# Kernel optimization log

Measured on AMD Instinct MI355X. Metric: run time of the kernel, lower is better.

Reference implementation:

```python
import jax, jax.numpy as jnp
import numpy as np

B, N, C, K = 2, 4096, 256, 64


def setup_inputs() -> dict:
    key = jax.random.key(0)
    k1, k2, k3, k4, k5, k6 = jax.random.split(key, 6)
    points = jax.random.normal(k1, (B, N, 3), dtype=jnp.float32)  # ~N(0,1) cloud
    point_features = jax.random.normal(k2, (B, N, C), dtype=jnp.float32)
    # proposals: centers inside the cloud, positive box dims, random yaw (unused by mask math)
    centers = jax.random.uniform(k3, (B, K, 3), minval=-1.0, maxval=1.0, dtype=jnp.float32)
    dims = jax.random.uniform(k4, (B, K, 3), minval=0.5, maxval=1.5, dtype=jnp.float32)
    ry = jax.random.uniform(k5, (B, K, 1), minval=-np.pi, maxval=np.pi, dtype=jnp.float32)
    proposals = jnp.concatenate([centers, dims, ry], axis=-1)  # (B,K,7)
    W1 = jax.random.normal(k6, (C, 256), dtype=jnp.float32) * (1.0 / np.sqrt(C))
    b1 = jnp.zeros((256,), dtype=jnp.float32)
    W2 = jax.random.normal(jax.random.fold_in(key, 7), (256, 256), dtype=jnp.float32) * (1.0 / 16.0)
    b2 = jnp.zeros((256,), dtype=jnp.float32)
    return {"points": points, "point_features": point_features, "proposals": proposals,
            "W1": W1, "b1": b1, "W2": W2, "b2": b2}


def reference(points, point_features, proposals, W1, b1, W2, b2):
    # points: (B,N,3), point_features: (B,N,C), proposals: (B,K,7)
    ctr = proposals[..., :3]                      # (B,K,3) cx,cy,cz
    half = proposals[..., 3:6] * 0.5              # (B,K,3) l/2,w/2,h/2
    lo = ctr - half                               # (B,K,3)
    hi = ctr + half
    # point-in-box mask (axis-aligned, strict inequalities as in source): (B,K,N)
    p = points[:, None, :, :]                     # (B,1,N,3)
    mask = jnp.all((p > lo[:, :, None, :]) & (p < hi[:, :, None, :]), axis=-1)
    any_in = jnp.any(mask, axis=-1)               # (B,K)
    # masked max-pool over points: (B,K,N,C) -> (B,K,C)
    neg_inf = jnp.asarray(-jnp.inf, point_features.dtype)
    masked = jnp.where(mask[..., None], point_features[:, None, :, :], neg_inf)
    pooled = jnp.max(masked, axis=2)
    pooled = jnp.where(any_in[..., None], pooled, 0.0)  # empty box -> zeros
    # fc: Linear(C,256) + ReLU + Linear(256,256) + ReLU
    h = jax.nn.relu(jnp.einsum('bkc,cd->bkd', pooled, W1) + b1)
    out = jax.nn.relu(jnp.einsum('bkd,de->bke', h, W2) + b2)
    return out
```

## Files before the change

### kernel.cpp

```cpp
#include <hip/hip_runtime.h>

#define Bn 2
#define Nn 4096
#define Cn 256
#define Kn 64
#define BK (Bn * Kn)

__global__ __launch_bounds__(256) void pool_partial_kernel(
    const float* __restrict__ points,
    const float* __restrict__ feats,
    const float* __restrict__ proposals,
    float* __restrict__ partial,
    int S)
{
    const int bk  = blockIdx.x;
    const int s   = blockIdx.y;
    const int b   = bk / Kn;
    const int tid = threadIdx.x;
    const int seg = Nn / S;
    const int n0  = s * seg;

    __shared__ int s_idx[4096];
    __shared__ int s_count;

    const float* prop = proposals + (size_t)bk * 7;
    const float cx = prop[0], cy = prop[1], cz = prop[2];
    const float hx = prop[3] * 0.5f, hy = prop[4] * 0.5f, hz = prop[5] * 0.5f;
    const float lox = cx - hx, loy = cy - hy, loz = cz - hz;
    const float hix = cx + hx, hiy = cy + hy, hiz = cz + hz;

    if (tid == 0) s_count = 0;
    __syncthreads();

    const float* pts = points + (size_t)b * Nn * 3;
    for (int n = n0 + tid; n < n0 + seg; n += 256) {
        const float px = pts[n * 3 + 0];
        const float py = pts[n * 3 + 1];
        const float pz = pts[n * 3 + 2];
        const bool in = (px > lox) & (px < hix) &
                        (py > loy) & (py < hiy) &
                        (pz > loz) & (pz < hiz);
        if (in) {
            const int pos = atomicAdd(&s_count, 1);
            s_idx[pos] = n;
        }
    }
    __syncthreads();
    const int count = s_count;

    const float* fb = feats + (size_t)b * Nn * Cn;
    float m = -INFINITY;
    int i = 0;
    for (; i + 8 <= count; i += 8) {
        const int a0 = s_idx[i + 0], a1 = s_idx[i + 1];
        const int a2 = s_idx[i + 2], a3 = s_idx[i + 3];
        const int a4 = s_idx[i + 4], a5 = s_idx[i + 5];
        const int a6 = s_idx[i + 6], a7 = s_idx[i + 7];
        const float f0 = fb[(size_t)a0 * Cn + tid];
        const float f1 = fb[(size_t)a1 * Cn + tid];
        const float f2 = fb[(size_t)a2 * Cn + tid];
        const float f3 = fb[(size_t)a3 * Cn + tid];
        const float f4 = fb[(size_t)a4 * Cn + tid];
        const float f5 = fb[(size_t)a5 * Cn + tid];
        const float f6 = fb[(size_t)a6 * Cn + tid];
        const float f7 = fb[(size_t)a7 * Cn + tid];
        m = fmaxf(m, fmaxf(fmaxf(fmaxf(f0, f1), fmaxf(f2, f3)),
                           fmaxf(fmaxf(f4, f5), fmaxf(f6, f7))));
    }
    for (; i < count; ++i) {
        m = fmaxf(m, fb[(size_t)s_idx[i] * Cn + tid]);
    }

    partial[((size_t)bk * S + s) * Cn + tid] = m;
}

__global__ __launch_bounds__(256) void reduce_mlp_kernel(
    const float* __restrict__ partial,
    const float* __restrict__ W1,
    const float* __restrict__ b1,
    const float* __restrict__ W2,
    const float* __restrict__ b2,
    float* __restrict__ out,
    int S)
{
    const int bk  = blockIdx.x;
    const int tid = threadIdx.x;

    __shared__ float s_vec[Cn];

    float m = -INFINITY;
    for (int s = 0; s < S; ++s) {
        m = fmaxf(m, partial[((size_t)bk * S + s) * Cn + tid]);
    }
    if (m == -INFINITY) m = 0.0f;
    s_vec[tid] = m;
    __syncthreads();

    float acc = b1[tid];
    #pragma unroll 16
    for (int c = 0; c < Cn; ++c) {
        acc = fmaf(s_vec[c], W1[c * 256 + tid], acc);
    }
    const float h = fmaxf(acc, 0.0f);
    __syncthreads();
    s_vec[tid] = h;
    __syncthreads();

    float acc2 = b2[tid];
    #pragma unroll 16
    for (int c = 0; c < 256; ++c) {
        acc2 = fmaf(s_vec[c], W2[c * 256 + tid], acc2);
    }
    out[(size_t)bk * 256 + tid] = fmaxf(acc2, 0.0f);
}

extern "C" void kernel_launch(void* const* d_in, const int* in_sizes, int n_in,
                              void* d_out, int out_size, void* d_ws, size_t ws_size,
                              hipStream_t stream) {
    const float* points    = (const float*)d_in[0];
    const float* feats     = (const float*)d_in[1];
    const float* proposals = (const float*)d_in[2];
    const float* W1        = (const float*)d_in[3];
    const float* b1        = (const float*)d_in[4];
    const float* W2        = (const float*)d_in[5];
    const float* b2        = (const float*)d_in[6];
    float* out             = (float*)d_out;
    float* partial         = (float*)d_ws;

    int S = 8;
    while (S > 1 && (size_t)BK * S * Cn * sizeof(float) > ws_size) S >>= 1;

    dim3 grid1(BK, S);
    pool_partial_kernel<<<grid1, 256, 0, stream>>>(points, feats, proposals, partial, S);
    reduce_mlp_kernel<<<BK, 256, 0, stream>>>(partial, W1, b1, W2, b2, out, S);
}
```

Measured before the change: 90.74 us.

## Fuse pooling and MLP into one 1024-thread kernel per proposal

```diff
diff --git a/kernel.cpp b/kernel.cpp
--- a/kernel.cpp
+++ b/kernel.cpp
@@ -5,23 +5,35 @@
 #define Cn 256
 #define Kn 64
 #define BK (Bn * Kn)
+#define NW 16
+#define BT 1024
 
-__global__ __launch_bounds__(256) void pool_partial_kernel(
+__device__ __forceinline__ float4 max4(float4 a, float4 b) {
+    return make_float4(fmaxf(a.x, b.x), fmaxf(a.y, b.y),
+                       fmaxf(a.z, b.z), fmaxf(a.w, b.w));
+}
+
+__global__ __launch_bounds__(BT) void fused_roi_kernel(
     const float* __restrict__ points,
     const float* __restrict__ feats,
     const float* __restrict__ proposals,
-    float* __restrict__ partial,
-    int S)
+    const float* __restrict__ W1,
+    const float* __restrict__ b1,
+    const float* __restrict__ W2,
+    const float* __restrict__ b2,
+    float* __restrict__ out)
 {
-    const int bk  = blockIdx.x;
-    const int s   = blockIdx.y;
-    const int b   = bk / Kn;
-    const int tid = threadIdx.x;
-    const int seg = Nn / S;
-    const int n0  = s * seg;
+    const int bk   = blockIdx.x;
+    const int b    = bk / Kn;
+    const int tid  = threadIdx.x;
+    const int w    = tid >> 6;
+    const int lane = tid & 63;
 
-    __shared__ int s_idx[4096];
-    __shared__ int s_count;
+    __shared__ int   s_idx[Nn];
+    __shared__ int   s_count;
+    __shared__ float s_part[NW][Cn];
+    __shared__ float s_vec[Cn];
+    __shared__ float s_red[4][Cn];
 
     const float* prop = proposals + (size_t)bk * 7;
     const float cx = prop[0], cy = prop[1], cz = prop[2];
@@ -33,7 +45,8 @@
     __syncthreads();
 
     const float* pts = points + (size_t)b * Nn * 3;
-    for (int n = n0 + tid; n < n0 + seg; n += 256) {
+    #pragma unroll
+    for (int n = tid; n < Nn; n += BT) {
         const float px = pts[n * 3 + 0];
         const float py = pts[n * 3 + 1];
         const float pz = pts[n * 3 + 2];
@@ -49,69 +62,79 @@
     const int count = s_count;
 
     const float* fb = feats + (size_t)b * Nn * Cn;
-    float m = -INFINITY;
-    int i = 0;
-    for (; i + 8 <= count; i += 8) {
-        const int a0 = s_idx[i + 0], a1 = s_idx[i + 1];
-        const int a2 = s_idx[i + 2], a3 = s_idx[i + 3];
-        const int a4 = s_idx[i + 4], a5 = s_idx[i + 5];
-        const int a6 = s_idx[i + 6], a7 = s_idx[i + 7];
-        const float f0 = fb[(size_t)a0 * Cn + tid];
-        const float f1 = fb[(size_t)a1 * Cn + tid];
-        const float f2 = fb[(size_t)a2 * Cn + tid];
-        const float f3 = fb[(size_t)a3 * Cn + tid];
-        const float f4 = fb[(size_t)a4 * Cn + tid];
-        const float f5 = fb[(size_t)a5 * Cn + tid];
-        const float f6 = fb[(size_t)a6 * Cn + tid];
-        const float f7 = fb[(size_t)a7 * Cn + tid];
-        m = fmaxf(m, fmaxf(fmaxf(fmaxf(f0, f1), fmaxf(f2, f3)),
-                           fmaxf(fmaxf(f4, f5), fmaxf(f6, f7))));
+    float4 mx = make_float4(-INFINITY, -INFINITY, -INFINITY, -INFINITY);
+    int i = w;
+    for (; i + 7 * NW < count; i += 8 * NW) {
+        const int a0 = s_idx[i + 0 * NW], a1 = s_idx[i + 1 * NW];
+        const int a2 = s_idx[i + 2 * NW], a3 = s_idx[i + 3 * NW];
+        const int a4 = s_idx[i + 4 * NW], a5 = s_idx[i + 5 * NW];
+        const int a6 = s_idx[i + 6 * NW], a7 = s_idx[i + 7 * NW];
+        const float4 f0 = *(const float4*)(fb + (size_t)a0 * Cn + lane * 4);
+        const float4 f1 = *(const float4*)(fb + (size_t)a1 * Cn + lane * 4);
+        const float4 f2 = *(const float4*)(fb + (size_t)a2 * Cn + lane * 4);
+        const float4 f3 = *(const float4*)(fb + (size_t)a3 * Cn + lane * 4);
+        const float4 f4 = *(const float4*)(fb + (size_t)a4 * Cn + lane * 4);
+        const float4 f5 = *(const float4*)(fb + (size_t)a5 * Cn + lane * 4);
+        const float4 f6 = *(const float4*)(fb + (size_t)a6 * Cn + lane * 4);
+        const float4 f7 = *(const float4*)(fb + (size_t)a7 * Cn + lane * 4);
+        mx = max4(mx, max4(max4(f0, f1), max4(f2, f3)));
+        mx = max4(mx, max4(max4(f4, f5), max4(f6, f7)));
     }
-    for (; i < count; ++i) {
-        m = fmaxf(m, fb[(size_t)s_idx[i] * Cn + tid]);
+    for (; i < count; i += NW) {
+        const int a = s_idx[i];
+        mx = max4(mx, *(const float4*)(fb + (size_t)a * Cn + lane * 4));
     }
-
-    partial[((size_t)bk * S + s) * Cn + tid] = m;
-}
-
-__global__ __launch_bounds__(256) void reduce_mlp_kernel(
-    const float* __restrict__ partial,
-    const float* __restrict__ W1,
-    const float* __restrict__ b1,
-    const float* __restrict__ W2,
-    const float* __restrict__ b2,
-    float* __restrict__ out,
-    int S)
-{
-    const int bk  = blockIdx.x;
-    const int tid = threadIdx.x;
-
-    __shared__ float s_vec[Cn];
-
-    float m = -INFINITY;
-    for (int s = 0; s < S; ++s) {
-        m = fmaxf(m, partial[((size_t)bk * S + s) * Cn + tid]);
-    }
-    if (m == -INFINITY) m = 0.0f;
-    s_vec[tid] = m;
+    *(float4*)&s_part[w][lane * 4] = mx;
     __syncthreads();
 
-    float acc = b1[tid];
-    #pragma unroll 16
-    for (int c = 0; c < Cn; ++c) {
-        acc = fmaf(s_vec[c], W1[c * 256 + tid], acc);
+    if (tid < Cn) {
+        float m = s_part[0][tid];
+        #pragma unroll
+        for (int k = 1; k < NW; ++k) m = fmaxf(m, s_part[k][tid]);
+        if (m == -INFINITY) m = 0.0f;
+        s_vec[tid] = m;
     }
-    const float h = fmaxf(acc, 0.0f);
-    __syncthreads();
-    s_vec[tid] = h;
     __syncthreads();
 
-    float acc2 = b2[tid];
-    #pragma unroll 16
-    for (int c = 0; c < 256; ++c) {
-        acc2 = fmaf(s_vec[c], W2[c * 256 + tid], acc2);
+    {
+        const int g = tid >> 8;
+        const int d = tid & 255;
+        const float* w1 = W1 + (size_t)(g * 64) * 256 + d;
+        const float* sv = s_vec + g * 64;
+        float acc = 0.0f;
+        #pragma unroll 16
+        for (int c = 0; c < 64; ++c) {
+            acc = fmaf(sv[c], w1[(size_t)c * 256], acc);
+        }
+        s_red[g][d] = acc;
     }
-    out[(size_t)bk * 256 + tid] = fmaxf(acc2, 0.0f);
+    __syncthreads();
+    if (tid < Cn) {
+        const float h = fmaxf(
+            b1[tid] + ((s_red[0][tid] + s_red[1][tid]) +
+                       (s_red[2][tid] + s_red[3][tid])), 0.0f);
+        s_vec[tid] = h;
+    }
+    __syncthreads();
+
+    {
+        const int g = tid >> 8;
+        const int d = tid & 255;
+        const float* w2 = W2 + (size_t)(g * 64) * 256 + d;
+        const float* sv = s_vec + g * 64;
+        float acc = 0.0f;
+        #pragma unroll 16
+        for (int c = 0; c < 64; ++c) {
+            acc = fmaf(sv[c], w2[(size_t)c * 256], acc);
+        }
+        s_red[g][d] = acc;
+    }
+    __syncthreads();
+    if (tid < Cn) {
+        out[(size_t)bk * 256 + tid] = fmaxf(
+            b2[tid] + ((s_red[0][tid] + s_red[1][tid]) +
+                       (s_red[2][tid] + s_red[3][tid])), 0.0f);
+    }
 }
 
 extern "C" void kernel_launch(void* const* d_in, const int* in_sizes, int n_in,
@@ -125,12 +148,8 @@
     const float* W2        = (const float*)d_in[5];
     const float* b2        = (const float*)d_in[6];
     float* out             = (float*)d_out;
-    float* partial         = (float*)d_ws;
+    (void)d_ws; (void)ws_size;
 
-    int S = 8;
-    while (S > 1 && (size_t)BK * S * Cn * sizeof(float) > ws_size) S >>= 1;
-
-    dim3 grid1(BK, S);
-    pool_partial_kernel<<<grid1, 256, 0, stream>>>(points, feats, proposals, partial, S);
-    reduce_mlp_kernel<<<BK, 256, 0, stream>>>(partial, W1, b1, W2, b2, out, S);
+    fused_roi_kernel<<<BK, BT, 0, stream>>>(points, feats, proposals,
+                                            W1, b1, W2, b2, out);
 }
```

After: 82.21 us. 9.4% less time.
